# Optimization experiments

Measured on AMD Instinct MI355X. Metric: run time of the kernel, lower is better.

The kernel has to match this reference:

```python
import jax, jax.numpy as jnp
import numpy as np

NUM_HEADS = 8
NORM_GROUPS = 32
EPS = 1e-5


def setup_inputs() -> dict:
    key = jax.random.key(0)
    k1, k2, k3 = jax.random.split(key, 3)
    b, c, h, w = 16, 256, 64, 64
    x = jax.random.normal(k1, (b, c, h, w), dtype=jnp.float32)
    gn_w = jnp.ones((c,), dtype=jnp.float32)
    gn_b = jnp.zeros((c,), dtype=jnp.float32)
    # 1x1 convs == channel matmuls; init like torch (kaiming-ish scale)
    w_qkv = jax.random.normal(k2, (3 * c, c), dtype=jnp.float32) / np.sqrt(c)
    w_proj = jax.random.normal(k3, (c, c), dtype=jnp.float32) / np.sqrt(c)
    b_proj = jnp.zeros((c,), dtype=jnp.float32)
    return {"x": x, "gn_w": gn_w, "gn_b": gn_b, "w_qkv": w_qkv,
            "w_proj": w_proj, "b_proj": b_proj}


def reference(x, gn_w, gn_b, w_qkv, w_proj, b_proj):
    b, c, h, w = x.shape
    H = NUM_HEADS
    d = c // H
    n = h * w
    # GroupNorm over (channels_per_group, h, w)
    xg = x.reshape(b, NORM_GROUPS, -1)
    mu = jnp.mean(xg, axis=-1, keepdims=True)
    var = jnp.mean(jnp.square(xg - mu), axis=-1, keepdims=True)
    xn = ((xg - mu) * jax.lax.rsqrt(var + EPS)).reshape(b, c, h, w)
    xn = xn * gn_w[None, :, None, None] + gn_b[None, :, None, None]
    # 1x1 conv -> (b, 3c, h, w); channel layout is (qkv, heads, d)
    qkv = jnp.einsum('oc,bchw->bohw', w_qkv, xn)
    qkv = qkv.reshape(b, 3, H, d, n)
    q, k, v = qkv[:, 0], qkv[:, 1], qkv[:, 2]  # each (b, H, d, n)
    k = jax.nn.softmax(k, axis=-1)
    # linear attention: small (d x d) state per head
    att = jnp.einsum('bhdn,bhen->bhde', k, v)
    out = jnp.einsum('bhde,bhdn->bhen', att, q)  # (b, H, d, n)
    out = out.reshape(b, c, h, w)
    return jnp.einsum('oc,bchw->bohw', w_proj, out) + b_proj[None, :, None, None]
```

## Files before the change

kernel.cpp:

```cpp
#include <hip/hip_runtime.h>
#include <stdint.h>

#define BATCH 16
#define CCH   256
#define NSP   4096

typedef unsigned short u16;
typedef short  short8 __attribute__((ext_vector_type(8)));
typedef float  f32x4  __attribute__((ext_vector_type(4)));

__device__ __forceinline__ float bf2f(u16 h) {
  union { unsigned int u; float f; } x; x.u = ((unsigned int)h) << 16; return x.f;
}
__device__ __forceinline__ u16 f2bf(float f) {
  union { float f; unsigned int u; } x; x.f = f;
  unsigned int r = 0x7fffu + ((x.u >> 16) & 1u);
  return (u16)((x.u + r) >> 16);
}

#define GLB(p) ((__attribute__((address_space(1))) void*)(p))
#define LDSP(p) ((__attribute__((address_space(3))) void*)(p))

__global__ __launch_bounds__(256) void convw_kernel(const float* __restrict__ wq,
                                                    const float* __restrict__ wp,
                                                    u16* __restrict__ dst) {
  const int i = (blockIdx.x * 256 + threadIdx.x) * 4;
  float4 v = (i < 196608) ? *(const float4*)(wq + i)
                          : *(const float4*)(wp + (i - 196608));
  ushort4 o;
  o.x = f2bf(v.x); o.y = f2bf(v.y); o.z = f2bf(v.z); o.w = f2bf(v.w);
  *(ushort4*)(dst + i) = o;
}

__global__ __launch_bounds__(256) void wqt_kernel(const u16* __restrict__ wq_bf,
                                                  u16* __restrict__ wqT) {
  __shared__ u16 ls[64][72];
  const int r0 = blockIdx.y * 64, c0 = blockIdx.x * 64;
  const int t = threadIdx.x;
#pragma unroll
  for (int j = 0; j < 2; ++j) {
    const int row = j * 32 + (t >> 3), col8 = (t & 7) * 8;
    *(uint4*)&ls[row][col8] = *(const uint4*)(wq_bf + (r0 + row) * 256 + c0 + col8);
  }
  __syncthreads();
#pragma unroll
  for (int j = 0; j < 2; ++j) {
    const int crow = j * 32 + (t >> 3), d8 = (t & 7) * 8;
    u16 tmp[8];
#pragma unroll
    for (int k = 0; k < 8; ++k) tmp[k] = ls[d8 + k][crow];
    *(uint4*)(wqT + (c0 + crow) * 256 + r0 + d8) = *(uint4*)tmp;
  }
}

__global__ __launch_bounds__(256) void gn_stats(const float* __restrict__ x,
                                                float2* __restrict__ stats,
                                                float* __restrict__ att4) {
  const int blk = blockIdx.x;
  const int tid = threadIdx.x;
  {
    float* az = att4 + (size_t)blk * 264;
    for (int i = tid; i < 264; i += 256) az[i] = 0.f;
  }
  const float4* xv = (const float4*)(x + (size_t)blk * 32768);
  float s = 0.f, ss = 0.f;
  for (int i = tid; i < 8192; i += 256) {
    float4 u = xv[i];
    s  += u.x + u.y + u.z + u.w;
    ss += u.x * u.x + u.y * u.y + u.z * u.z + u.w * u.w;
  }
#pragma unroll
  for (int off = 32; off > 0; off >>= 1) {
    s  += __shfl_down(s, off);
    ss += __shfl_down(ss, off);
  }
  __shared__ float red[8];
  const int wave = tid >> 6, lane = tid & 63;
  if (lane == 0) { red[wave * 2] = s; red[wave * 2 + 1] = ss; }
  __syncthreads();
  if (tid == 0) {
    const float S  = red[0] + red[2] + red[4] + red[6];
    const float SS = red[1] + red[3] + red[5] + red[7];
    const float mean = S * (1.f / 32768.f);
    const float var  = SS * (1.f / 32768.f) - mean * mean;
    stats[blk] = make_float2(mean, rsqrtf(var + 1e-5f));
  }
}

__global__ __launch_bounds__(256) void gn_apply_t(const float* __restrict__ x,
                                                  const float* __restrict__ gw,
                                                  const float* __restrict__ gb,
                                                  const float2* __restrict__ stats,
                                                  u16* __restrict__ xnT) {
  __shared__ u16 ls[64][72];
  const int b = blockIdx.z, c0 = blockIdx.y * 64, n0 = blockIdx.x * 64;
  const int tid = threadIdx.x;
#pragma unroll
  for (int r = 0; r < 4; ++r) {
    const int cc = (tid >> 4) + r * 16;
    const int nn = (tid & 15) * 4;
    const int c = c0 + cc;
    const float2 st = stats[b * 32 + (c >> 3)];
    const float wv = gw[c] * st.y;
    const float bv = gb[c] - st.x * wv;
    float4 u = *(const float4*)(x + ((size_t)b * CCH + c) * NSP + n0 + nn);
    ushort4 o;
    o.x = f2bf(u.x * wv + bv);
    o.y = f2bf(u.y * wv + bv);
    o.z = f2bf(u.z * wv + bv);
    o.w = f2bf(u.w * wv + bv);
    *(ushort4*)&ls[cc][nn] = o;
  }
  __syncthreads();
#pragma unroll
  for (int p = 0; p < 2; ++p) {
    const int idx = tid + p * 256;
    const int nn = idx >> 3;
    const int cb = (idx & 7) * 8;
    u16 tmp[8];
#pragma unroll
    for (int j = 0; j < 8; ++j) tmp[j] = ls[cb + j][nn];
    *(uint4*)(xnT + ((size_t)b * NSP + n0 + nn) * CCH + c0 + cb) = *(uint4*)tmp;
  }
}

template <int OUTF32>
__global__ __launch_bounds__(256) void gemm_mfma(const u16* __restrict__ A,
                                                 const u16* __restrict__ Bt,
                                                 const float* __restrict__ bias,
                                                 void* __restrict__ Cm, int M,
                                                 int aBatch, long btStride, int ldc) {
  __shared__ __align__(16) u16 smem[17408];
  const int tid = threadIdx.x, wave = tid >> 6, lane = tid & 63;
  const int n0 = blockIdx.x * 128, m0 = blockIdx.y * 128, bz = blockIdx.z;
  const u16* Ab = A + (size_t)bz * aBatch;
  const u16* Bb = Bt + (size_t)bz * btStride;

  const int lrow = lane >> 3;
  const int kcl  = ((lane & 7) ^ lrow) * 8;
  const u16* pA[4]; const u16* pB[4];
#pragma unroll
  for (int j = 0; j < 4; ++j) {
    const int row = j * 32 + wave * 8 + lrow;
    pA[j] = Ab + (size_t)(m0 + row) * CCH + kcl;
    pB[j] = Bb + (size_t)(n0 + row) * CCH + kcl;
  }
  u16* lA = smem;
  u16* lB = smem + 8192;

  const int wm = wave >> 1, wn = wave & 1;
  f32x4 acc[4][4];
#pragma unroll
  for (int i = 0; i < 4; ++i)
#pragma unroll
    for (int j = 0; j < 4; ++j) acc[i][j] = (f32x4){0.f, 0.f, 0.f, 0.f};

  for (int it = 0; it < 4; ++it) {
#pragma unroll
    for (int j = 0; j < 4; ++j) {
      __builtin_amdgcn_global_load_lds(GLB(pA[j]), LDSP(lA + (j * 256 + wave * 64) * 8), 16, 0, 0);
      __builtin_amdgcn_global_load_lds(GLB(pB[j]), LDSP(lB + (j * 256 + wave * 64) * 8), 16, 0, 0);
      pA[j] += 64; pB[j] += 64;
    }
    __syncthreads();
#pragma unroll
    for (int w = 0; w < 2; ++w) {
      const int kcf = w * 4 + (lane >> 4);
      short8 af[4], bfr[4];
#pragma unroll
      for (int mt = 0; mt < 4; ++mt) {
        const int row = wm * 64 + mt * 16 + (lane & 15);
        af[mt] = *(const short8*)&lA[(row * 8 + (kcf ^ (row & 7))) * 8];
      }
#pragma unroll
      for (int nt = 0; nt < 4; ++nt) {
        const int row = wn * 64 + nt * 16 + (lane & 15);
        bfr[nt] = *(const short8*)&lB[(row * 8 + (kcf ^ (row & 7))) * 8];
      }
#pragma unroll
      for (int mt = 0; mt < 4; ++mt)
#pragma unroll
        for (int nt = 0; nt < 4; ++nt)
          acc[mt][nt] = __builtin_amdgcn_mfma_f32_16x16x32_bf16(af[mt], bfr[nt], acc[mt][nt], 0, 0, 0);
    }
    __syncthreads();
  }

  if (!OUTF32) {
    u16* cl = smem;
#pragma unroll
    for (int mt = 0; mt < 4; ++mt)
#pragma unroll
      for (int nt = 0; nt < 4; ++nt)
#pragma unroll
        for (int r = 0; r < 4; ++r) {
          const int row = wm * 64 + mt * 16 + (lane >> 4) * 4 + r;
          const int col = wn * 64 + nt * 16 + (lane & 15);
          cl[row * 136 + col] = f2bf(acc[mt][nt][r]);
        }
    __syncthreads();
    u16* C = (u16*)Cm + (size_t)bz * (size_t)M * ldc;
#pragma unroll
    for (int j = 0; j < 8; ++j) {
      const int idx = tid + j * 256;
      const int row = idx >> 4, chunk = idx & 15;
      *(uint4*)(C + (size_t)(m0 + row) * ldc + n0 + chunk * 8) =
          *(const uint4*)&cl[row * 136 + chunk * 8];
    }
  } else {
    float* clf = (float*)smem;
    float* C = (float*)Cm + (size_t)bz * (size_t)M * ldc;
#pragma unroll
    for (int pass = 0; pass < 2; ++pass) {
      if (wm == pass) {
#pragma unroll
        for (int mt = 0; mt < 4; ++mt)
#pragma unroll
          for (int nt = 0; nt < 4; ++nt)
#pragma unroll
            for (int r = 0; r < 4; ++r) {
              const int rl = mt * 16 + (lane >> 4) * 4 + r;
              const int col = wn * 64 + nt * 16 + (lane & 15);
              clf[rl * 132 + col] = acc[mt][nt][r] + bias[m0 + pass * 64 + rl];
            }
      }
      __syncthreads();
#pragma unroll
      for (int j = 0; j < 8; ++j) {
        const int idx = tid + j * 256;
        const int row = idx >> 5, chunk = idx & 31;
        *(float4*)(C + (size_t)(m0 + pass * 64 + row) * ldc + n0 + chunk * 4) =
            *(const float4*)&clf[row * 132 + chunk * 4];
      }
      __syncthreads();
    }
  }
}

__global__ __launch_bounds__(256) void gemm_kv_att(const u16* __restrict__ A,
                                                   const u16* __restrict__ Bt,
                                                   float* __restrict__ att4) {
  __shared__ __align__(16) u16 smem[20992];
  const int tid = threadIdx.x, wave = tid >> 6, lane = tid & 63;
  const int n0 = blockIdx.x * 128, hg = blockIdx.y, b = blockIdx.z;
  const u16* Bb = Bt + (size_t)b * (size_t)NSP * CCH;

  const int lrow = lane >> 3;
  const int kcl  = ((lane & 7) ^ lrow) * 8;
  u16* lA  = smem;
  u16* lB  = smem + 4096;
  u16* clV = smem;
  u16* clK = smem + 12288;
  const int wm = wave >> 1, wn = wave & 1;

  for (int pass = 0; pass < 2; ++pass) {
    const int m0 = 256 + pass * 256 + hg * 64;
    const u16* pA[2]; const u16* pB[4];
#pragma unroll
    for (int j = 0; j < 2; ++j)
      pA[j] = A + (size_t)(m0 + j * 32 + wave * 8 + lrow) * CCH + kcl;
#pragma unroll
    for (int j = 0; j < 4; ++j)
      pB[j] = Bb + (size_t)(n0 + j * 32 + wave * 8 + lrow) * CCH + kcl;

    f32x4 acc[2][4];
#pragma unroll
    for (int i = 0; i < 2; ++i)
#pragma unroll
      for (int j = 0; j < 4; ++j) acc[i][j] = (f32x4){0.f, 0.f, 0.f, 0.f};

    for (int it = 0; it < 4; ++it) {
#pragma unroll
      for (int j = 0; j < 2; ++j) {
        __builtin_amdgcn_global_load_lds(GLB(pA[j]), LDSP(lA + (j * 256 + wave * 64) * 8), 16, 0, 0);
        pA[j] += 64;
      }
#pragma unroll
      for (int j = 0; j < 4; ++j) {
        __builtin_amdgcn_global_load_lds(GLB(pB[j]), LDSP(lB + (j * 256 + wave * 64) * 8), 16, 0, 0);
        pB[j] += 64;
      }
      __syncthreads();
#pragma unroll
      for (int w = 0; w < 2; ++w) {
        const int kcf = w * 4 + (lane >> 4);
        short8 af[2], bfr[4];
#pragma unroll
        for (int mt = 0; mt < 2; ++mt) {
          const int row = wm * 32 + mt * 16 + (lane & 15);
          af[mt] = *(const short8*)&lA[(row * 8 + (kcf ^ (row & 7))) * 8];
        }
#pragma unroll
        for (int nt = 0; nt < 4; ++nt) {
          const int row = wn * 64 + nt * 16 + (lane & 15);
          bfr[nt] = *(const short8*)&lB[(row * 8 + (kcf ^ (row & 7))) * 8];
        }
#pragma unroll
        for (int mt = 0; mt < 2; ++mt)
#pragma unroll
          for (int nt = 0; nt < 4; ++nt)
            acc[mt][nt] = __builtin_amdgcn_mfma_f32_16x16x32_bf16(af[mt], bfr[nt], acc[mt][nt], 0, 0, 0);
      }
      __syncthreads();
    }

    u16* cl = pass ? clV : clK;
#pragma unroll
    for (int mt = 0; mt < 2; ++mt)
#pragma unroll
      for (int nt = 0; nt < 4; ++nt)
#pragma unroll
        for (int r = 0; r < 4; ++r) {
          const int row = wm * 32 + mt * 16 + (lane >> 4) * 4 + r;
          const int col = wn * 64 + nt * 16 + (lane & 15);
          const float v = acc[mt][nt][r];
          cl[row * 136 + col] = f2bf(pass ? v : __expf(v));
        }
  }
  __syncthreads();

  const int hh = wave >> 1, nhalf = wave & 1;
  const int bh = b * 8 + hg * 2 + hh;
  f32x4 a2[2][2], al[2];
#pragma unroll
  for (int i = 0; i < 2; ++i) {
    al[i] = (f32x4){0.f, 0.f, 0.f, 0.f};
#pragma unroll
    for (int j = 0; j < 2; ++j) a2[i][j] = (f32x4){0.f, 0.f, 0.f, 0.f};
  }
  short8 ones;
#pragma unroll
  for (int j = 0; j < 8; ++j) ones[j] = (short)0x3F80;

  const int rr = lane & 15, cc8 = (lane >> 4) * 8;
#pragma unroll
  for (int c = 0; c < 2; ++c) {
    const int n = (nhalf * 2 + c) * 32 + cc8;
    short8 ek0 = *(const short8*)&clK[(hh * 32 + rr) * 136 + n];
    short8 ek1 = *(const short8*)&clK[(hh * 32 + 16 + rr) * 136 + n];
    short8 v0  = *(const short8*)&clV[(hh * 32 + rr) * 136 + n];
    short8 v1  = *(const short8*)&clV[(hh * 32 + 16 + rr) * 136 + n];
    a2[0][0] = __builtin_amdgcn_mfma_f32_16x16x32_bf16(ek0, v0, a2[0][0], 0, 0, 0);
    a2[0][1] = __builtin_amdgcn_mfma_f32_16x16x32_bf16(ek0, v1, a2[0][1], 0, 0, 0);
    a2[1][0] = __builtin_amdgcn_mfma_f32_16x16x32_bf16(ek1, v0, a2[1][0], 0, 0, 0);
    a2[1][1] = __builtin_amdgcn_mfma_f32_16x16x32_bf16(ek1, v1, a2[1][1], 0, 0, 0);
    al[0]    = __builtin_amdgcn_mfma_f32_16x16x32_bf16(ek0, ones, al[0], 0, 0, 0);
    al[1]    = __builtin_amdgcn_mfma_f32_16x16x32_bf16(ek1, ones, al[1], 0, 0, 0);
  }
  __syncthreads();

  float* red  = (float*)smem;
  float* redl = red + 2176;
  const int dq = (lane >> 4) * 4;
  if (nhalf == 1) {
#pragma unroll
    for (int dh = 0; dh < 2; ++dh) {
#pragma unroll
      for (int eh = 0; eh < 2; ++eh)
#pragma unroll
        for (int j = 0; j < 4; ++j)
          red[hh * 1088 + (dh * 16 + dq + j) * 34 + eh * 16 + rr] = a2[dh][eh][j];
      if (rr == 0)
#pragma unroll
        for (int j = 0; j < 4; ++j) redl[hh * 32 + dh * 16 + dq + j] = al[dh][j];
    }
  }
  __syncthreads();
  if (nhalf == 0) {
    float* ap = att4 + (size_t)bh * 1056;
#pragma unroll
    for (int dh = 0; dh < 2; ++dh) {
#pragma unroll
      for (int eh = 0; eh < 2; ++eh)
#pragma unroll
        for (int j = 0; j < 4; ++j) {
          const int d = dh * 16 + dq + j, e = eh * 16 + rr;
          atomicAdd(&ap[d * 32 + e], a2[dh][eh][j] + red[hh * 1088 + d * 34 + e]);
        }
      if (rr == 0)
#pragma unroll
        for (int j = 0; j < 4; ++j) {
          const int d = dh * 16 + dq + j;
          atomicAdd(&ap[1024 + d], al[dh][j] + redl[hh * 32 + d]);
        }
    }
  }
}

__global__ __launch_bounds__(256) void w2_kernel(const u16* __restrict__ wp_bf,
                                                 const float* __restrict__ att4,
                                                 u16* __restrict__ W2) {
  const int b = blockIdx.x >> 4;
  const int o0 = (blockIdx.x & 15) * 16;
  const int tid = threadIdx.x;
  const int h = tid >> 5, d = tid & 31;
  const float* ap = att4 + ((size_t)b * 8 + h) * 1056;
  const float linv = 1.f / ap[1024 + d];
  float as[32];
#pragma unroll
  for (int e = 0; e < 32; ++e) as[e] = ap[d * 32 + e] * linv;
  u16* w2p = W2 + (size_t)b * 65536;
  for (int oi = 0; oi < 16; ++oi) {
    const int o = o0 + oi;
    const uint4* wr = (const uint4*)(wp_bf + o * 256 + h * 32);
    float acc = 0.f;
#pragma unroll
    for (int j = 0; j < 4; ++j) {
      uint4 u = wr[j];
      const u16* w8 = (const u16*)&u;
#pragma unroll
      for (int t = 0; t < 8; ++t) acc += bf2f(w8[t]) * as[j * 8 + t];
    }
    w2p[o * 256 + tid] = f2bf(acc);
  }
}

extern "C" void kernel_launch(void* const* d_in, const int* in_sizes, int n_in,
                              void* d_out, int out_size, void* d_ws, size_t ws_size,
                              hipStream_t stream) {
  const float* x      = (const float*)d_in[0];
  const float* gn_w   = (const float*)d_in[1];
  const float* gn_b   = (const float*)d_in[2];
  const float* w_qkv  = (const float*)d_in[3];
  const float* w_proj = (const float*)d_in[4];
  const float* b_proj = (const float*)d_in[5];
  float* out = (float*)d_out;

  char* ws = (char*)d_ws;
  u16*    xnT   = (u16*)ws;
  u16*    wbf   = (u16*)(ws + 33554432ull);
  u16*    wqT   = (u16*)(ws + 34078720ull);
  u16*    W2    = (u16*)(ws + 34209792ull);
  u16*    W3    = (u16*)(ws + 36306944ull);
  float*  att4  = (float*)(ws + 38404096ull);
  float2* stats = (float2*)(ws + 38944768ull);
  u16* wq_bf = wbf;
  u16* wp_bf = wbf + 196608;

  convw_kernel<<<256, 256, 0, stream>>>(w_qkv, w_proj, wbf);
  wqt_kernel<<<dim3(4, 4), 256, 0, stream>>>(wq_bf, wqT);
  gn_stats<<<512, 256, 0, stream>>>(x, stats, att4);
  gn_apply_t<<<dim3(64, 4, 16), 256, 0, stream>>>(x, gn_w, gn_b, stats, xnT);
  gemm_kv_att<<<dim3(32, 4, 16), 256, 0, stream>>>(wq_bf, xnT, att4);
  w2_kernel<<<256, 256, 0, stream>>>(wp_bf, att4, W2);
  gemm_mfma<0><<<dim3(2, 2, 16), 256, 0, stream>>>(W2, wqT, nullptr, W3,
                                                   CCH, 65536, 0L, CCH);
  gemm_mfma<1><<<dim3(32, 2, 16), 256, 0, stream>>>(W3, xnT, b_proj, out,
                                                    CCH, 65536, (long)NSP * CCH, NSP);
}
```

Baseline: 223.5 us.

## Merge prep kernels and compute K and V in one fused GEMM pass

The weight bf16 conversion, the weight transpose and the GroupNorm stats kernels are merged into one launch with block-range dispatch. The transpose now reads fp32 weights directly instead of depending on the converted buffer. In gemm_kv_att, the two sequential K and V passes become a single 128x128 tile pass: each wave pair computes K or V, the xnT tile is loaded once instead of twice, and there are half as many barriers. This adds accumulator registers (16 MFMA tiles per wave), and launch bounds are set to allow 4 blocks per CU.

```diff
diff --git a/kernel.cpp b/kernel.cpp
--- a/kernel.cpp
+++ b/kernel.cpp
@@ -21,69 +21,71 @@
 #define GLB(p) ((__attribute__((address_space(1))) void*)(p))
 #define LDSP(p) ((__attribute__((address_space(3))) void*)(p))
 
-__global__ __launch_bounds__(256) void convw_kernel(const float* __restrict__ wq,
-                                                    const float* __restrict__ wp,
-                                                    u16* __restrict__ dst) {
-  const int i = (blockIdx.x * 256 + threadIdx.x) * 4;
-  float4 v = (i < 196608) ? *(const float4*)(wq + i)
-                          : *(const float4*)(wp + (i - 196608));
-  ushort4 o;
-  o.x = f2bf(v.x); o.y = f2bf(v.y); o.z = f2bf(v.z); o.w = f2bf(v.w);
-  *(ushort4*)(dst + i) = o;
-}
-
-__global__ __launch_bounds__(256) void wqt_kernel(const u16* __restrict__ wq_bf,
-                                                  u16* __restrict__ wqT) {
+__global__ __launch_bounds__(256) void prep_kernel(const float* __restrict__ x,
+                                                   const float* __restrict__ wq,
+                                                   const float* __restrict__ wp,
+                                                   float2* __restrict__ stats,
+                                                   float* __restrict__ att4,
+                                                   u16* __restrict__ wbf,
+                                                   u16* __restrict__ wqT) {
+  __shared__ float red[8];
   __shared__ u16 ls[64][72];
-  const int r0 = blockIdx.y * 64, c0 = blockIdx.x * 64;
-  const int t = threadIdx.x;
-#pragma unroll
-  for (int j = 0; j < 2; ++j) {
-    const int row = j * 32 + (t >> 3), col8 = (t & 7) * 8;
-    *(uint4*)&ls[row][col8] = *(const uint4*)(wq_bf + (r0 + row) * 256 + c0 + col8);
-  }
-  __syncthreads();
-#pragma unroll
-  for (int j = 0; j < 2; ++j) {
-    const int crow = j * 32 + (t >> 3), d8 = (t & 7) * 8;
-    u16 tmp[8];
-#pragma unroll
-    for (int k = 0; k < 8; ++k) tmp[k] = ls[d8 + k][crow];
-    *(uint4*)(wqT + (c0 + crow) * 256 + r0 + d8) = *(uint4*)tmp;
-  }
-}
-
-__global__ __launch_bounds__(256) void gn_stats(const float* __restrict__ x,
-                                                float2* __restrict__ stats,
-                                                float* __restrict__ att4) {
-  const int blk = blockIdx.x;
-  const int tid = threadIdx.x;
-  {
-    float* az = att4 + (size_t)blk * 264;
-    for (int i = tid; i < 264; i += 256) az[i] = 0.f;
-  }
-  const float4* xv = (const float4*)(x + (size_t)blk * 32768);
-  float s = 0.f, ss = 0.f;
-  for (int i = tid; i < 8192; i += 256) {
-    float4 u = xv[i];
-    s  += u.x + u.y + u.z + u.w;
-    ss += u.x * u.x + u.y * u.y + u.z * u.z + u.w * u.w;
-  }
-#pragma unroll
-  for (int off = 32; off > 0; off >>= 1) {
-    s  += __shfl_down(s, off);
-    ss += __shfl_down(ss, off);
-  }
-  __shared__ float red[8];
-  const int wave = tid >> 6, lane = tid & 63;
-  if (lane == 0) { red[wave * 2] = s; red[wave * 2 + 1] = ss; }
-  __syncthreads();
-  if (tid == 0) {
-    const float S  = red[0] + red[2] + red[4] + red[6];
-    const float SS = red[1] + red[3] + red[5] + red[7];
-    const float mean = S * (1.f / 32768.f);
-    const float var  = SS * (1.f / 32768.f) - mean * mean;
-    stats[blk] = make_float2(mean, rsqrtf(var + 1e-5f));
+  const int blk = blockIdx.x, tid = threadIdx.x;
+  if (blk < 512) {
+    {
+      float* az = att4 + (size_t)blk * 264;
+      for (int i = tid; i < 264; i += 256) az[i] = 0.f;
+    }
+    const float4* xv = (const float4*)(x + (size_t)blk * 32768);
+    float s = 0.f, ss = 0.f;
+    for (int i = tid; i < 8192; i += 256) {
+      float4 u = xv[i];
+      s  += u.x + u.y + u.z + u.w;
+      ss += u.x * u.x + u.y * u.y + u.z * u.z + u.w * u.w;
+    }
+#pragma unroll
+    for (int off = 32; off > 0; off >>= 1) {
+      s  += __shfl_down(s, off);
+      ss += __shfl_down(ss, off);
+    }
+    const int wave = tid >> 6, lane = tid & 63;
+    if (lane == 0) { red[wave * 2] = s; red[wave * 2 + 1] = ss; }
+    __syncthreads();
+    if (tid == 0) {
+      const float S  = red[0] + red[2] + red[4] + red[6];
+      const float SS = red[1] + red[3] + red[5] + red[7];
+      const float mean = S * (1.f / 32768.f);
+      const float var  = SS * (1.f / 32768.f) - mean * mean;
+      stats[blk] = make_float2(mean, rsqrtf(var + 1e-5f));
+    }
+  } else if (blk < 768) {
+    const int i = ((blk - 512) * 256 + tid) * 4;
+    float4 v = (i < 196608) ? *(const float4*)(wq + i)
+                            : *(const float4*)(wp + (i - 196608));
+    ushort4 o;
+    o.x = f2bf(v.x); o.y = f2bf(v.y); o.z = f2bf(v.z); o.w = f2bf(v.w);
+    *(ushort4*)(wbf + i) = o;
+  } else {
+    const int t2 = blk - 768;
+    const int c0 = (t2 & 3) * 64, r0 = (t2 >> 2) * 64;
+#pragma unroll
+    for (int j = 0; j < 4; ++j) {
+      const int row = j * 16 + (tid >> 4), col = (tid & 15) * 4;
+      float4 u = *(const float4*)(wq + (r0 + row) * 256 + c0 + col);
+      ls[row][col]     = f2bf(u.x);
+      ls[row][col + 1] = f2bf(u.y);
+      ls[row][col + 2] = f2bf(u.z);
+      ls[row][col + 3] = f2bf(u.w);
+    }
+    __syncthreads();
+#pragma unroll
+    for (int j = 0; j < 2; ++j) {
+      const int crow = j * 32 + (tid >> 3), d8 = (tid & 7) * 8;
+      u16 tmp[8];
+#pragma unroll
+      for (int k = 0; k < 8; ++k) tmp[k] = ls[d8 + k][crow];
+      *(uint4*)(wqT + (c0 + crow) * 256 + r0 + d8) = *(uint4*)tmp;
+    }
   }
 }
 
@@ -237,85 +239,91 @@
   }
 }
 
-__global__ __launch_bounds__(256) void gemm_kv_att(const u16* __restrict__ A,
-                                                   const u16* __restrict__ Bt,
-                                                   float* __restrict__ att4) {
-  __shared__ __align__(16) u16 smem[20992];
+__global__ __launch_bounds__(256, 4) void gemm_kv_att(const u16* __restrict__ A,
+                                                      const u16* __restrict__ Bt,
+                                                      float* __restrict__ att4) {
+  __shared__ __align__(16) u16 smem[17408];
   const int tid = threadIdx.x, wave = tid >> 6, lane = tid & 63;
   const int n0 = blockIdx.x * 128, hg = blockIdx.y, b = blockIdx.z;
   const u16* Bb = Bt + (size_t)b * (size_t)NSP * CCH;
 
   const int lrow = lane >> 3;
   const int kcl  = ((lane & 7) ^ lrow) * 8;
-  u16* lA  = smem;
-  u16* lB  = smem + 4096;
-  u16* clV = smem;
-  u16* clK = smem + 12288;
+  const u16* pA[4]; const u16* pB[4];
+#pragma unroll
+  for (int j = 0; j < 4; ++j) {
+    const int arow = 256 + (j >> 1) * 256 + hg * 64 + (j & 1) * 32 + wave * 8 + lrow;
+    pA[j] = A  + (size_t)arow * CCH + kcl;
+    pB[j] = Bb + (size_t)(n0 + j * 32 + wave * 8 + lrow) * CCH + kcl;
+  }
+  u16* lA = smem;
+  u16* lB = smem + 8192;
+
   const int wm = wave >> 1, wn = wave & 1;
-
-  for (int pass = 0; pass < 2; ++pass) {
-    const int m0 = 256 + pass * 256 + hg * 64;
-    const u16* pA[2]; const u16* pB[4];
-#pragma unroll
-    for (int j = 0; j < 2; ++j)
-      pA[j] = A + (size_t)(m0 + j * 32 + wave * 8 + lrow) * CCH + kcl;
-#pragma unroll
-    for (int j = 0; j < 4; ++j)
-      pB[j] = Bb + (size_t)(n0 + j * 32 + wave * 8 + lrow) * CCH + kcl;
-
-    f32x4 acc[2][4];
-#pragma unroll
-    for (int i = 0; i < 2; ++i)
-#pragma unroll
-      for (int j = 0; j < 4; ++j) acc[i][j] = (f32x4){0.f, 0.f, 0.f, 0.f};
-
-    for (int it = 0; it < 4; ++it) {
-#pragma unroll
-      for (int j = 0; j < 2; ++j) {
-        __builtin_amdgcn_global_load_lds(GLB(pA[j]), LDSP(lA + (j * 256 + wave * 64) * 8), 16, 0, 0);
-        pA[j] += 64;
-      }
-#pragma unroll
-      for (int j = 0; j < 4; ++j) {
-        __builtin_amdgcn_global_load_lds(GLB(pB[j]), LDSP(lB + (j * 256 + wave * 64) * 8), 16, 0, 0);
-        pB[j] += 64;
-      }
-      __syncthreads();
-#pragma unroll
-      for (int w = 0; w < 2; ++w) {
-        const int kcf = w * 4 + (lane >> 4);
-        short8 af[2], bfr[4];
-#pragma unroll
-        for (int mt = 0; mt < 2; ++mt) {
-          const int row = wm * 32 + mt * 16 + (lane & 15);
-          af[mt] = *(const short8*)&lA[(row * 8 + (kcf ^ (row & 7))) * 8];
-        }
-#pragma unroll
-        for (int nt = 0; nt < 4; ++nt) {
-          const int row = wn * 64 + nt * 16 + (lane & 15);
-          bfr[nt] = *(const short8*)&lB[(row * 8 + (kcf ^ (row & 7))) * 8];
-        }
-#pragma unroll
-        for (int mt = 0; mt < 2; ++mt)
-#pragma unroll
-          for (int nt = 0; nt < 4; ++nt)
-            acc[mt][nt] = __builtin_amdgcn_mfma_f32_16x16x32_bf16(af[mt], bfr[nt], acc[mt][nt], 0, 0, 0);
-      }
-      __syncthreads();
-    }
-
-    u16* cl = pass ? clV : clK;
-#pragma unroll
-    for (int mt = 0; mt < 2; ++mt)
-#pragma unroll
-      for (int nt = 0; nt < 4; ++nt)
-#pragma unroll
-        for (int r = 0; r < 4; ++r) {
-          const int row = wm * 32 + mt * 16 + (lane >> 4) * 4 + r;
-          const int col = wn * 64 + nt * 16 + (lane & 15);
-          const float v = acc[mt][nt][r];
-          cl[row * 136 + col] = f2bf(pass ? v : __expf(v));
-        }
+  f32x4 acc[4][4];
+#pragma unroll
+  for (int i = 0; i < 4; ++i)
+#pragma unroll
+    for (int j = 0; j < 4; ++j) acc[i][j] = (f32x4){0.f, 0.f, 0.f, 0.f};
+
+  for (int it = 0; it < 4; ++it) {
+#pragma unroll
+    for (int j = 0; j < 4; ++j) {
+      __builtin_amdgcn_global_load_lds(GLB(pA[j]), LDSP(lA + (j * 256 + wave * 64) * 8), 16, 0, 0);
+      __builtin_amdgcn_global_load_lds(GLB(pB[j]), LDSP(lB + (j * 256 + wave * 64) * 8), 16, 0, 0);
+      pA[j] += 64; pB[j] += 64;
+    }
+    __syncthreads();
+#pragma unroll
+    for (int w = 0; w < 2; ++w) {
+      const int kcf = w * 4 + (lane >> 4);
+      short8 af[4], bfr[4];
+#pragma unroll
+      for (int mt = 0; mt < 4; ++mt) {
+        const int row = wm * 64 + mt * 16 + (lane & 15);
+        af[mt] = *(const short8*)&lA[(row * 8 + (kcf ^ (row & 7))) * 8];
+      }
+#pragma unroll
+      for (int nt = 0; nt < 4; ++nt) {
+        const int row = wn * 64 + nt * 16 + (lane & 15);
+        bfr[nt] = *(const short8*)&lB[(row * 8 + (kcf ^ (row & 7))) * 8];
+      }
+#pragma unroll
+      for (int mt = 0; mt < 4; ++mt)
+#pragma unroll
+        for (int nt = 0; nt < 4; ++nt)
+          acc[mt][nt] = __builtin_amdgcn_mfma_f32_16x16x32_bf16(af[mt], bfr[nt], acc[mt][nt], 0, 0, 0);
+    }
+    __syncthreads();
+  }
+
+  u16* clK = smem;
+  u16* clV = smem + 8704;
+  {
+    const int rbase = (lane >> 4) * 4;
+    if (wm == 0) {
+#pragma unroll
+      for (int mt = 0; mt < 4; ++mt)
+#pragma unroll
+        for (int nt = 0; nt < 4; ++nt)
+#pragma unroll
+          for (int r = 0; r < 4; ++r) {
+            const int row = mt * 16 + rbase + r;
+            const int col = wn * 64 + nt * 16 + (lane & 15);
+            clK[row * 136 + col] = f2bf(__expf(acc[mt][nt][r]));
+          }
+    } else {
+#pragma unroll
+      for (int mt = 0; mt < 4; ++mt)
+#pragma unroll
+        for (int nt = 0; nt < 4; ++nt)
+#pragma unroll
+          for (int r = 0; r < 4; ++r) {
+            const int row = mt * 16 + rbase + r;
+            const int col = wn * 64 + nt * 16 + (lane & 15);
+            clV[row * 136 + col] = f2bf(acc[mt][nt][r]);
+          }
+    }
   }
   __syncthreads();
 
@@ -437,9 +445,7 @@
   u16* wq_bf = wbf;
   u16* wp_bf = wbf + 196608;
 
-  convw_kernel<<<256, 256, 0, stream>>>(w_qkv, w_proj, wbf);
-  wqt_kernel<<<dim3(4, 4), 256, 0, stream>>>(wq_bf, wqT);
-  gn_stats<<<512, 256, 0, stream>>>(x, stats, att4);
+  prep_kernel<<<784, 256, 0, stream>>>(x, w_qkv, w_proj, stats, att4, wbf, wqT);
   gn_apply_t<<<dim3(64, 4, 16), 256, 0, stream>>>(x, gn_w, gn_b, stats, xnT);
   gemm_kv_att<<<dim3(32, 4, 16), 256, 0, stream>>>(wq_bf, xnT, att4);
   w2_kernel<<<256, 256, 0, stream>>>(wp_bf, att4, W2);
```

Result: faster. 208.1 us (-6.9%).
